# Kernel optimization log

Measured on AMD Instinct MI355X. Metric: run time of the kernel, lower is better.

The kernel has to match this reference:

```python
import jax, jax.numpy as jnp
import numpy as np

N, E, D_IN, D_OUT = 50000, 600000, 128, 128
BETA, ALPHA = 0.4, 0.6


def setup_inputs() -> dict:
    key = jax.random.key(0)
    ks = jax.random.split(key, 8)
    def xavier(k, shape):
        std = (2.0 / (shape[0] + shape[1])) ** 0.5
        return jax.random.normal(k, shape, jnp.float32) * std
    x = jax.random.normal(ks[0], (N, D_IN), jnp.float32)
    edge_index = jax.random.randint(ks[1], (2, E), 0, N, jnp.int32)
    Wq = xavier(ks[2], (D_IN, D_OUT))
    Wk = xavier(ks[3], (D_IN, D_OUT))
    Wv = xavier(ks[4], (D_IN, D_IN))
    W_gcn = xavier(ks[5], (D_IN, D_IN))   # GCNConv linear weight [out, in]
    b_gcn = jnp.zeros((D_IN,), jnp.float32)
    W_lin = xavier(ks[6], (D_OUT, D_IN))  # nn.Linear weight [out, in]
    b_lin = jnp.zeros((D_OUT,), jnp.float32)
    return {"x": x, "edge_index": edge_index, "Wq": Wq, "Wk": Wk, "Wv": Wv,
            "W_gcn": W_gcn, "b_gcn": b_gcn, "W_lin": W_lin, "b_lin": b_lin}


def gcn_conv(x, edge_index, W, b):
    # PyG GCNConv default: add self-loops, symmetric deg^-1/2 normalization.
    n = x.shape[0]
    loops = jnp.arange(n, dtype=edge_index.dtype)
    src = jnp.concatenate([edge_index[0], loops])
    dst = jnp.concatenate([edge_index[1], loops])
    deg = jax.ops.segment_sum(jnp.ones_like(dst, jnp.float32), dst, num_segments=n)
    d_inv_sqrt = jax.lax.rsqrt(deg)  # deg >= 1 thanks to self-loops
    norm = d_inv_sqrt[src] * d_inv_sqrt[dst]  # [E+N]
    xw = x @ W.T                               # [N, d]
    out = jax.ops.segment_sum(xw[src] * norm[:, None], dst, num_segments=n)
    return out + b


def reference(x, edge_index, Wq, Wk, Wv, W_gcn, b_gcn, W_lin, b_lin):
    n, d_in = x.shape
    q = x @ Wq
    q_hat = q / jnp.linalg.norm(q)  # Frobenius norm
    k = x @ Wk
    k_hat = k / jnp.linalg.norm(k)
    v = x @ Wv
    # qk = q_hat @ (k_hat^T @ 1) / in_channels  -> [n]
    qk = (q_hat @ k_hat.sum(axis=0)) / d_in
    # D = diag(1 + qk); inverse of diagonal is elementwise reciprocal
    scale = 1.0 / (1.0 + qk)
    attn = v + (q_hat @ (k_hat.T @ v)) / d_in  # [n, d_in]
    Z = BETA * scale[:, None] * attn + (1.0 - BETA) * x
    gcn = gcn_conv(x, edge_index, W_gcn, b_gcn)
    # self.dropout(gcn) result is discarded in the source -> no-op
    Z_out = (1.0 - ALPHA) * Z + ALPHA * gcn
    return Z_out @ W_lin.T + b_lin
```

## Files before the change

### kernel.cpp

```cpp
#include <hip/hip_runtime.h>
#include <hip/hip_fp16.h>
#include <cstdint>
#include <cstddef>

#define D 128
typedef unsigned short u16;
typedef short bf16x8 __attribute__((ext_vector_type(8)));
typedef float f32x4 __attribute__((ext_vector_type(4)));

__device__ __forceinline__ u16 f2b(float f) {
    uint32_t u = __float_as_uint(f);
    return (u16)((u + 0x7FFFu + ((u >> 16) & 1u)) >> 16);
}
__device__ __forceinline__ float b2f(u16 b) {
    return __uint_as_float(((uint32_t)b) << 16);
}

#define SWZ(r, k) ((k) ^ (((r) & 7) << 3))

__global__ void k_prep(const float* __restrict__ Wq, const float* __restrict__ Wk,
                       const float* __restrict__ Wv, const float* __restrict__ Wg,
                       const float* __restrict__ bg, const float* __restrict__ Wl,
                       const float* __restrict__ bl,
                       u16* __restrict__ Bcatb, float* __restrict__ biasout)
{
    const int b = blockIdx.x;
    const int t = threadIdx.x;
    if (b < 640) {
        const int strip = b >> 7, n = b & 127;
        float val;
        if (strip == 0) {
            val = Wq[t * D + n];
        } else if (strip == 1) {
            val = Wk[t * D + n];
        } else if (strip == 2) {
            float s = 0.f;
#pragma unroll 8
            for (int m = 0; m < D; ++m) s += Wv[t * D + m] * Wl[n * D + m];
            val = s;
        } else if (strip == 3) {
            val = Wl[n * D + t];
        } else {
            float s = 0.f;
#pragma unroll 8
            for (int m = 0; m < D; ++m) s += Wl[n * D + m] * Wg[m * D + t];
            val = 0.6f * s;
        }
        Bcatb[(size_t)b * D + t] = f2b(val);
    } else {
        float s = 0.f;
#pragma unroll 8
        for (int m = 0; m < D; ++m) s += bg[m] * Wl[t * D + m];
        biasout[t] = bl[t] + 0.6f * s;
    }
}

__global__ void k_init(int* __restrict__ cnt, int M)
{
    const int i = blockIdx.x * 256 + threadIdx.x;
    if (i < M) cnt[i] = 0;
}

__global__ void k_hist(const int* __restrict__ dst, int* __restrict__ cnt,
                       int* __restrict__ epos, int E)
{
    const int e = blockIdx.x * 256 + threadIdx.x;
    if (e < E) epos[e] = atomicAdd(&cnt[dst[e]], 1);
}

__global__ __launch_bounds__(1024) void k_scan1(const int* __restrict__ cnt,
                                                int* __restrict__ offs,
                                                int* __restrict__ bsum,
                                                float* __restrict__ dinv, int M)
{
    __shared__ int wsum[16];
    const int t = threadIdx.x, lane = t & 63, w = t >> 6;
    const int i = blockIdx.x * 1024 + t;
    const int v = (i < M) ? cnt[i] : 0;
    if (i < M) dinv[i] = rsqrtf((float)(v + 1));
    int s = v;
    for (int off = 1; off < 64; off <<= 1) {
        int n = __shfl_up(s, off);
        if (lane >= off) s += n;
    }
    if (lane == 63) wsum[w] = s;
    __syncthreads();
    if (w == 0) {
        int ss = (lane < 16) ? wsum[lane] : 0;
        for (int off = 1; off < 16; off <<= 1) {
            int n = __shfl_up(ss, off);
            if (lane >= off) ss += n;
        }
        if (lane < 16) wsum[lane] = ss;
    }
    __syncthreads();
    const int woff = (w == 0) ? 0 : wsum[w - 1];
    if (i < M) offs[i] = woff + s - v;
    if (t == 1023) bsum[blockIdx.x] = wsum[15];
}

__global__ void k_scanB(int* __restrict__ bsum, int nb)
{
    const int t = threadIdx.x;
    int v = (t < nb) ? bsum[t] : 0;
    int s = v;
    for (int off = 1; off < 64; off <<= 1) {
        int n = __shfl_up(s, off);
        if (t >= off) s += n;
    }
    if (t < nb) bsum[t] = s - v;
}

__global__ void k_scan2(const int* __restrict__ bsum, int* __restrict__ offs, int M)
{
    const int i = blockIdx.x * 256 + threadIdx.x;
    if (i < M) offs[i] += bsum[i >> 10];
}

__global__ void k_fill(const int* __restrict__ src, const int* __restrict__ dst,
                       const int* __restrict__ epos,
                       const float* __restrict__ dinv,
                       const int* __restrict__ offs,
                       uint32_t* __restrict__ cpk, int E)
{
    const int e = blockIdx.x * 256 + threadIdx.x;
    if (e < E) {
        const int s = src[e], d = dst[e];
        const int pos = offs[d] + epos[e];
        const float w = dinv[s] * dinv[d];
        const u16 hb = __half_as_ushort(__float2half(w));
        cpk[pos] = (uint32_t)(u16)s | ((uint32_t)hb << 16);
    }
}

__global__ __launch_bounds__(256) void k_gemm5(const float* __restrict__ x,
                                               const u16* __restrict__ Bcatb,
                                               u16* __restrict__ outbase,
                                               int M, size_t NQ)
{
    __shared__ u16 As[64 * D];
    __shared__ u16 Bs[64 * D];
    const int t = threadIdx.x;
    const int row0 = blockIdx.x * 64;
    const int n0 = blockIdx.y * 64;

#pragma unroll
    for (int p = 0; p < 4; ++p) {
        const int flat = t + 256 * p;
        const int r = flat >> 4, kg = flat & 15;
        int gr = row0 + r; if (gr > M - 1) gr = M - 1;
        const float4 f0 = *(const float4*)(x + (size_t)gr * D + kg * 8);
        const float4 f1 = *(const float4*)(x + (size_t)gr * D + kg * 8 + 4);
        u16 rr[8] = {f2b(f0.x), f2b(f0.y), f2b(f0.z), f2b(f0.w),
                     f2b(f1.x), f2b(f1.y), f2b(f1.z), f2b(f1.w)};
        *(uint4*)(As + r * D + SWZ(r, kg * 8)) = *(const uint4*)rr;
    }
#pragma unroll
    for (int p = 0; p < 4; ++p) {
        const int flat = t + 256 * p;
        const int r = flat >> 4, kg = flat & 15;
        const uint4 v = *(const uint4*)(Bcatb + (size_t)(n0 + r) * D + kg * 8);
        *(uint4*)(Bs + r * D + SWZ(r, kg * 8)) = v;
    }
    __syncthreads();

    const int lane = t & 63, w = t >> 6;
    const int wr = (w >> 1) * 32, wc = (w & 1) * 32;
    const int fr = lane & 15, kg = lane >> 4;

    f32x4 acc[2][2] = {};
#pragma unroll
    for (int ks = 0; ks < 4; ++ks) {
        const int kb = ks * 32 + kg * 8;
        bf16x8 a[2], b[2];
#pragma unroll
        for (int i = 0; i < 2; ++i) {
            const int r = wr + 16 * i + fr;
            a[i] = *(const bf16x8*)(As + r * D + SWZ(r, kb));
        }
#pragma unroll
        for (int j = 0; j < 2; ++j) {
            const int r = wc + 16 * j + fr;
            b[j] = *(const bf16x8*)(Bs + r * D + SWZ(r, kb));
        }
#pragma unroll
        for (int i = 0; i < 2; ++i)
#pragma unroll
            for (int j = 0; j < 2; ++j)
                acc[i][j] = __builtin_amdgcn_mfma_f32_16x16x32_bf16(a[i], b[j], acc[i][j], 0, 0, 0);
    }

    const int mat = n0 >> 7, col0 = n0 & 127;
    u16* outp = outbase + (size_t)mat * NQ;
#pragma unroll
    for (int i = 0; i < 2; ++i) {
#pragma unroll
        for (int reg = 0; reg < 4; ++reg) {
            const int r = row0 + wr + 16 * i + kg * 4 + reg;
            if (r < M) {
#pragma unroll
                for (int j = 0; j < 2; ++j) {
                    const int c = col0 + wc + 16 * j + fr;
                    outp[(size_t)r * D + c] = f2b(acc[i][j][reg]);
                }
            }
        }
    }
}

__global__ __launch_bounds__(256) void k_stats(const u16* __restrict__ qb,
                                               const u16* __restrict__ kb,
                                               float* __restrict__ psq,
                                               float* __restrict__ psk,
                                               float* __restrict__ pks, size_t NQ)
{
    __shared__ float lks[D];
    __shared__ float red[8];
    const int t = threadIdx.x;
    if (t < D) lks[t] = 0.f;
    __syncthreads();
    float sq = 0.f, sk = 0.f;
    float kc[8] = {0.f, 0.f, 0.f, 0.f, 0.f, 0.f, 0.f, 0.f};
    const size_t step = (size_t)gridDim.x * 256 * 8;
    const int cb = (t * 8) & 127;
    for (size_t i = ((size_t)blockIdx.x * 256 + t) * 8; i < NQ; i += step) {
        const uint4 qv = *(const uint4*)(qb + i);
        const uint4 kv = *(const uint4*)(kb + i);
        const u16* qp = (const u16*)&qv;
        const u16* kp = (const u16*)&kv;
#pragma unroll
        for (int jj = 0; jj < 8; ++jj) {
            const float q = b2f(qp[jj]); sq += q * q;
            const float k = b2f(kp[jj]); sk += k * k; kc[jj] += k;
        }
    }
#pragma unroll
    for (int jj = 0; jj < 8; ++jj) atomicAdd(&lks[cb + jj], kc[jj]);
    for (int off = 32; off > 0; off >>= 1) {
        sq += __shfl_down(sq, off);
        sk += __shfl_down(sk, off);
    }
    const int w = t >> 6;
    if ((t & 63) == 0) { red[w] = sq; red[4 + w] = sk; }
    __syncthreads();
    if (t == 0) psq[blockIdx.x] = red[0] + red[1] + red[2] + red[3];
    if (t == 64) psk[blockIdx.x] = red[4] + red[5] + red[6] + red[7];
    if (t < D) pks[(size_t)blockIdx.x * D + t] = lks[t];
}

__global__ __launch_bounds__(256) void k_ktv(const u16* __restrict__ kb,
                                             const u16* __restrict__ vWb,
                                             float* __restrict__ part, int M)
{
    __shared__ u16 kT[D * 64];
    __shared__ u16 vT[D * 64];
    const int t = threadIdx.x;
    const int P = (int)gridDim.x;
    const int chunk = (M + P - 1) / P;
    const int rbeg = blockIdx.x * chunk;
    const int rend = min(rbeg + chunk, M);

    const int lane = t & 63, w = t >> 6;
    const int fr = lane & 15, kg = lane >> 4;

    f32x4 acc[2][8] = {};

    for (int r0 = rbeg; r0 < rend; r0 += 64) {
#pragma unroll
        for (int p = 0; p < 4; ++p) {
            const int flat = t + 256 * p;
            const int rr = flat & 63, cg = flat >> 6;
            const int gr = r0 + rr;
            uint4 kv = make_uint4(0, 0, 0, 0), vv = make_uint4(0, 0, 0, 0);
            if (gr < rend) {
                kv = *(const uint4*)(kb + (size_t)gr * D + cg * 8);
                vv = *(const uint4*)(vWb + (size_t)gr * D + cg * 8);
            }
            const u16* kp = (const u16*)&kv;
            const u16* vp = (const u16*)&vv;
#pragma unroll
            for (int jj = 0; jj < 8; ++jj) {
                const int c = cg * 8 + jj;
                const int ri = rr ^ ((c & 7) << 3);
                kT[c * 64 + ri] = kp[jj];
                vT[c * 64 + ri] = vp[jj];
            }
        }
        __syncthreads();
#pragma unroll
        for (int ks = 0; ks < 2; ++ks) {
            const int rb = ks * 32 + kg * 8;
            bf16x8 a[2], b[8];
#pragma unroll
            for (int i = 0; i < 2; ++i) {
                const int m = w * 32 + 16 * i + fr;
                a[i] = *(const bf16x8*)(kT + m * 64 + (rb ^ ((m & 7) << 3)));
            }
#pragma unroll
            for (int j = 0; j < 8; ++j) {
                const int n = 16 * j + fr;
                b[j] = *(const bf16x8*)(vT + n * 64 + (rb ^ ((n & 7) << 3)));
            }
#pragma unroll
            for (int i = 0; i < 2; ++i)
#pragma unroll
                for (int j = 0; j < 8; ++j)
                    acc[i][j] = __builtin_amdgcn_mfma_f32_16x16x32_bf16(a[i], b[j], acc[i][j], 0, 0, 0);
        }
        __syncthreads();
    }
    float* pp = part + (size_t)blockIdx.x * (D * D);
#pragma unroll
    for (int i = 0; i < 2; ++i)
#pragma unroll
        for (int reg = 0; reg < 4; ++reg) {
            const int m = w * 32 + 16 * i + kg * 4 + reg;
#pragma unroll
            for (int j = 0; j < 8; ++j)
                pp[(size_t)m * D + 16 * j + fr] = acc[i][j][reg];
        }
}

__global__ void k_redC(const float* __restrict__ part, float* __restrict__ Craw, int P)
{
    const int e = blockIdx.x * 256 + threadIdx.x;
    float s0 = 0.f, s1 = 0.f, s2 = 0.f, s3 = 0.f,
          s4 = 0.f, s5 = 0.f, s6 = 0.f, s7 = 0.f;
    int p = 0;
    for (; p + 8 <= P; p += 8) {
        s0 += part[(size_t)(p + 0) * (D * D) + e];
        s1 += part[(size_t)(p + 1) * (D * D) + e];
        s2 += part[(size_t)(p + 2) * (D * D) + e];
        s3 += part[(size_t)(p + 3) * (D * D) + e];
        s4 += part[(size_t)(p + 4) * (D * D) + e];
        s5 += part[(size_t)(p + 5) * (D * D) + e];
        s6 += part[(size_t)(p + 6) * (D * D) + e];
        s7 += part[(size_t)(p + 7) * (D * D) + e];
    }
    for (; p < P; ++p) s0 += part[(size_t)p * (D * D) + e];
    Craw[e] = ((s0 + s1) + (s2 + s3)) + ((s4 + s5) + (s6 + s7));
}

__global__ __launch_bounds__(1024) void k_scalc3t(const float* __restrict__ psq,
                                                  const float* __restrict__ psk,
                                                  const float* __restrict__ pks,
                                                  const float* __restrict__ Craw,
                                                  float* __restrict__ kq,
                                                  u16* __restrict__ C3b, int NBLK)
{
    __shared__ float lpart[8][D];
    __shared__ float wred[16];
    __shared__ float invS;
    const int t = threadIdx.x;
    const int col = t & 127, grp = t >> 7;
    float s = 0.f;
#pragma unroll 8
    for (int bq = grp; bq < NBLK; bq += 8) s += pks[(size_t)bq * D + col];
    lpart[grp][col] = s;
    const int w = t >> 6, lane = t & 63;
    float v = 0.f;
    if (t < NBLK) v = psq[t];
    else if (t < 2 * NBLK) v = psk[t - NBLK];
    for (int off = 32; off > 0; off >>= 1) v += __shfl_down(v, off);
    if (lane == 0 && w < 8) wred[w] = v;
    __syncthreads();
    if (t == 0) {
        const float sq = wred[0] + wred[1] + wred[2] + wred[3];
        const float sk = wred[4] + wred[5] + wred[6] + wred[7];
        invS = 1.0f / (sqrtf(sq) * sqrtf(sk) * 128.0f);
    }
    float ks = 0.f;
    if (t < D) {
#pragma unroll
        for (int g = 0; g < 8; ++g) ks += lpart[g][t];
    }
    __syncthreads();
    const float inv = invS;
    if (t < D) kq[t] = ks * inv;
#pragma unroll
    for (int i = 0; i < 16; ++i) {
        const int e = t + 1024 * i;
        C3b[e] = f2b(Craw[(size_t)(e & 127) * D + (e >> 7)] * inv);
    }
}

__global__ __launch_bounds__(256) void k_final(const u16* __restrict__ qb,
                                               const u16* __restrict__ C3b,
                                               const u16* __restrict__ vWb,
                                               const u16* __restrict__ xWb,
                                               const u16* __restrict__ ub,
                                               const int* __restrict__ cnt,
                                               const float* __restrict__ kq,
                                               const float* __restrict__ biasout,
                                               float* __restrict__ out, int M)
{
    __shared__ u16 As[64 * D];
    __shared__ u16 Bs[D * D];
    __shared__ float scaleS[64];
    const int t = threadIdx.x;
    const int row0 = blockIdx.x * 64;

#pragma unroll
    for (int p = 0; p < 4; ++p) {
        const int flat = t + 256 * p;
        const int r = flat >> 4, kg2 = flat & 15;
        int gr = row0 + r; if (gr > M - 1) gr = M - 1;
        const uint4 v = *(const uint4*)(qb + (size_t)gr * D + kg2 * 8);
        *(uint4*)(As + r * D + SWZ(r, kg2 * 8)) = v;
    }
#pragma unroll
    for (int p = 0; p < 8; ++p) {
        const int flat = t + 256 * p;
        const int r = flat >> 4, kg2 = flat & 15;
        const uint4 v = *(const uint4*)(C3b + (size_t)r * D + kg2 * 8);
        *(uint4*)(Bs + r * D + SWZ(r, kg2 * 8)) = v;
    }
    __syncthreads();

    {
        const int rr = t >> 2, qq = t & 3;
        float s = 0.f;
#pragma unroll
        for (int i = 0; i < 4; ++i) {
            const int kk = qq * 32 + i * 8;
            const bf16x8 a = *(const bf16x8*)(As + rr * D + SWZ(rr, kk));
            const u16* ap = (const u16*)&a;
#pragma unroll
            for (int jj = 0; jj < 8; ++jj) s += b2f(ap[jj]) * kq[kk + jj];
        }
        s += __shfl_xor(s, 1);
        s += __shfl_xor(s, 2);
        if (qq == 0) scaleS[rr] = 0.16f / (1.0f + s);
    }

    const int lane = t & 63, w = t >> 6;
    const int fr = lane & 15, kg = lane >> 4;

    f32x4 acc[8] = {};
#pragma unroll
    for (int ks = 0; ks < 4; ++ks) {
        const int kb2 = ks * 32 + kg * 8;
        const int r = w * 16 + fr;
        const bf16x8 a = *(const bf16x8*)(As + r * D + SWZ(r, kb2));
#pragma unroll
        for (int j = 0; j < 8; ++j) {
            const int n = 16 * j + fr;
            const bf16x8 b = *(const bf16x8*)(Bs + n * D + SWZ(n, kb2));
            acc[j] = __builtin_amdgcn_mfma_f32_16x16x32_bf16(a, b, acc[j], 0, 0, 0);
        }
    }
    __syncthreads();

#pragma unroll
    for (int reg = 0; reg < 4; ++reg) {
        const int rr = w * 16 + kg * 4 + reg;
        const int r = row0 + rr;
        if (r < M) {
            const float rc = scaleS[rr];
            const float sc = 1.0f / (float)(cnt[r] + 1);
#pragma unroll
            for (int j = 0; j < 8; ++j) {
                const int c = 16 * j + fr;
                const size_t idx = (size_t)r * D + c;
                out[idx] = rc * (b2f(vWb[idx]) + acc[j][reg]) + 0.24f * b2f(xWb[idx])
                         + biasout[c] + sc * b2f(ub[idx]);
            }
        }
    }
}

__global__ __launch_bounds__(256) void k_gather(const int* __restrict__ offs,
                                                const int* __restrict__ cnt,
                                                const uint32_t* __restrict__ cpk,
                                                const u16* __restrict__ ub,
                                                float* __restrict__ out, int M)
{
    const int t = threadIdx.x;
    const int w = t >> 6, lane = t & 63;
    const int d = blockIdx.x * 4 + w;
    if (d >= M) return;
    const int g = lane >> 4, sub = lane & 15;
    const int beg = offs[d];
    const int n = cnt[d];
    if (n == 0) return;
    const int end = beg + n;
    float acc[8] = {};
    for (int j0 = beg; j0 < end; j0 += 8) {
        const int j1 = j0 + g, j2 = j0 + 4 + g;
        int s1 = 0, s2 = 0;
        float w1 = 0.f, w2 = 0.f;
        if (j1 < end) {
            const uint32_t p = cpk[j1];
            s1 = (int)(p & 0xFFFFu);
            w1 = __half2float(__ushort_as_half((u16)(p >> 16)));
        }
        if (j2 < end) {
            const uint32_t p = cpk[j2];
            s2 = (int)(p & 0xFFFFu);
            w2 = __half2float(__ushort_as_half((u16)(p >> 16)));
        }
        const uint4 r1 = *(const uint4*)(ub + (size_t)s1 * D + sub * 8);
        const uint4 r2 = *(const uint4*)(ub + (size_t)s2 * D + sub * 8);
        const u16* p1 = (const u16*)&r1;
        const u16* p2 = (const u16*)&r2;
#pragma unroll
        for (int i = 0; i < 8; ++i) acc[i] += w1 * b2f(p1[i]) + w2 * b2f(p2[i]);
    }
#pragma unroll
    for (int i = 0; i < 8; ++i) {
        acc[i] += __shfl_xor(acc[i], 16);
        acc[i] += __shfl_xor(acc[i], 32);
    }
    if (g == 0) {
        float* o = out + (size_t)d * D + sub * 8;
        float4 o0 = *(float4*)o, o1 = *(float4*)(o + 4);
        o0.x += acc[0]; o0.y += acc[1]; o0.z += acc[2]; o0.w += acc[3];
        o1.x += acc[4]; o1.y += acc[5]; o1.z += acc[6]; o1.w += acc[7];
        *(float4*)o = o0; *(float4*)(o + 4) = o1;
    }
}

extern "C" void kernel_launch(void* const* d_in, const int* in_sizes, int n_in,
                              void* d_out, int out_size, void* d_ws, size_t ws_size,
                              hipStream_t stream)
{
    const float* x  = (const float*)d_in[0];
    const int*   ei = (const int*)d_in[1];
    const float* Wq = (const float*)d_in[2];
    const float* Wk = (const float*)d_in[3];
    const float* Wv = (const float*)d_in[4];
    const float* Wg = (const float*)d_in[5];
    const float* bg = (const float*)d_in[6];
    const float* Wl = (const float*)d_in[7];
    const float* bl = (const float*)d_in[8];

    const int M = in_sizes[0] / D;
    const int E = in_sizes[1] / 2;
    const size_t NQ = (size_t)M * D;
    const int P = 192;
    const int SB = 256;
    const int NB = (M + 1023) / 1024;

    char* base = (char*)d_ws;
    auto alloc = [&](size_t bytes) -> char* {
        char* p = base; base += (bytes + 63) & ~(size_t)63; return p;
    };
    float* part    = (float*)alloc((size_t)P * D * D * 4);
    float* Craw    = (float*)alloc(D * D * 4);
    float* dinv    = (float*)alloc((size_t)M * 4);
    float* psq     = (float*)alloc(SB * 4);
    float* psk     = (float*)alloc(SB * 4);
    float* pks     = (float*)alloc((size_t)SB * D * 4);
    float* kq      = (float*)alloc(D * 4);
    float* biasout = (float*)alloc(D * 4);
    int*   cnt     = (int*)alloc((size_t)M * 4);
    int*   offs    = (int*)alloc((size_t)M * 4);
    int*   bsum    = (int*)alloc(64 * 4);
    int*   epos    = (int*)alloc((size_t)E * 4);
    uint32_t* cpk  = (uint32_t*)alloc((size_t)E * 4);
    u16*   Bcatb   = (u16*)alloc((size_t)640 * D * 2);
    u16*   C3b     = (u16*)alloc(D * D * 2);
    u16*   qb      = (u16*)alloc(NQ * 2);
    u16*   kb      = (u16*)alloc(NQ * 2);
    u16*   vWb     = (u16*)alloc(NQ * 2);
    u16*   xWb     = (u16*)alloc(NQ * 2);
    u16*   ub      = (u16*)alloc(NQ * 2);
    (void)kb; (void)vWb; (void)xWb;

    float* out = (float*)d_out;

    k_prep<<<dim3(641), dim3(128), 0, stream>>>(Wq, Wk, Wv, Wg, bg, Wl, bl, Bcatb, biasout);
    k_init<<<(M + 255) / 256, 256, 0, stream>>>(cnt, M);
    k_hist<<<(E + 255) / 256, 256, 0, stream>>>(ei + E, cnt, epos, E);
    k_scan1<<<NB, 1024, 0, stream>>>(cnt, offs, bsum, dinv, M);
    k_scanB<<<1, 64, 0, stream>>>(bsum, NB);
    k_scan2<<<(M + 255) / 256, 256, 0, stream>>>(bsum, offs, M);
    k_fill<<<(E + 255) / 256, 256, 0, stream>>>(ei, ei + E, epos, dinv, offs, cpk, E);

    k_gemm5<<<dim3((M + 63) / 64, 10), 256, 0, stream>>>(x, Bcatb, qb, M, NQ);
    k_stats<<<SB, 256, 0, stream>>>(qb, kb, psq, psk, pks, NQ);
    k_ktv<<<P, 256, 0, stream>>>(kb, vWb, part, M);
    k_redC<<<64, 256, 0, stream>>>(part, Craw, P);
    k_scalc3t<<<1, 1024, 0, stream>>>(psq, psk, pks, Craw, kq, C3b, SB);

    k_final<<<(M + 63) / 64, 256, 0, stream>>>(qb, C3b, vWb, xWb, ub, cnt, kq, biasout, out, M);
    k_gather<<<(M + 3) / 4, 256, 0, stream>>>(offs, cnt, cpk, ub, out, M);
}
```

Before: 208.4 us.

## Fuse Q/K norm stats into projection GEMM and loop all column tiles per block

The projection GEMM now launches one block per 64-row tile. Each block loops over all ten 64-column chunks of the concatenated weight matrix, double-buffering the weight tiles in shared memory, so the x tile is loaded and converted once instead of ten times. The Frobenius-norm sums and K column sums are accumulated in the GEMM epilogue, with shared atomics for the column sums. That removes the separate stats kernel and its re-read of q and k. The tradeoffs are fewer, longer blocks with more shared memory and serialized column work, shared-atomic contention, and a final reduction over many more per-block partials.

```diff
diff --git a/kernel.cpp b/kernel.cpp
--- a/kernel.cpp
+++ b/kernel.cpp
@@ -136,13 +136,19 @@
 __global__ __launch_bounds__(256) void k_gemm5(const float* __restrict__ x,
                                                const u16* __restrict__ Bcatb,
                                                u16* __restrict__ outbase,
+                                               float* __restrict__ psq,
+                                               float* __restrict__ psk,
+                                               float* __restrict__ pks,
                                                int M, size_t NQ)
 {
     __shared__ u16 As[64 * D];
-    __shared__ u16 Bs[64 * D];
+    __shared__ u16 Bs[2][64 * D];
+    __shared__ float lks[D];
+    __shared__ float red[8];
     const int t = threadIdx.x;
     const int row0 = blockIdx.x * 64;
-    const int n0 = blockIdx.y * 64;
+
+    if (t < D) lks[t] = 0.f;
 
 #pragma unroll
     for (int p = 0; p < 4; ++p) {
@@ -159,88 +165,84 @@
     for (int p = 0; p < 4; ++p) {
         const int flat = t + 256 * p;
         const int r = flat >> 4, kg = flat & 15;
-        const uint4 v = *(const uint4*)(Bcatb + (size_t)(n0 + r) * D + kg * 8);
-        *(uint4*)(Bs + r * D + SWZ(r, kg * 8)) = v;
+        const uint4 v = *(const uint4*)(Bcatb + (size_t)r * D + kg * 8);
+        *(uint4*)(Bs[0] + r * D + SWZ(r, kg * 8)) = v;
     }
     __syncthreads();
 
     const int lane = t & 63, w = t >> 6;
     const int wr = (w >> 1) * 32, wc = (w & 1) * 32;
-    const int fr = lane & 15, kg = lane >> 4;
-
-    f32x4 acc[2][2] = {};
-#pragma unroll
-    for (int ks = 0; ks < 4; ++ks) {
-        const int kb = ks * 32 + kg * 8;
-        bf16x8 a[2], b[2];
+    const int fr = lane & 15, kg2 = lane >> 4;
+
+    float sq = 0.f, sk = 0.f;
+
+    for (int c = 0; c < 10; ++c) {
+        const int cur = c & 1;
+        if (c < 9) {
+#pragma unroll
+            for (int p = 0; p < 4; ++p) {
+                const int flat = t + 256 * p;
+                const int r = flat >> 4, kg = flat & 15;
+                const uint4 v = *(const uint4*)(Bcatb + (size_t)((c + 1) * 64 + r) * D + kg * 8);
+                *(uint4*)(Bs[cur ^ 1] + r * D + SWZ(r, kg * 8)) = v;
+            }
+        }
+
+        f32x4 acc[2][2] = {};
+#pragma unroll
+        for (int ks = 0; ks < 4; ++ks) {
+            const int kb = ks * 32 + kg2 * 8;
+            bf16x8 a[2], b[2];
+#pragma unroll
+            for (int i = 0; i < 2; ++i) {
+                const int r = wr + 16 * i + fr;
+                a[i] = *(const bf16x8*)(As + r * D + SWZ(r, kb));
+            }
+#pragma unroll
+            for (int j = 0; j < 2; ++j) {
+                const int r = wc + 16 * j + fr;
+                b[j] = *(const bf16x8*)(Bs[cur] + r * D + SWZ(r, kb));
+            }
+#pragma unroll
+            for (int i = 0; i < 2; ++i)
+#pragma unroll
+                for (int j = 0; j < 2; ++j)
+                    acc[i][j] = __builtin_amdgcn_mfma_f32_16x16x32_bf16(a[i], b[j], acc[i][j], 0, 0, 0);
+        }
+
+        const int mat = c >> 1, col0 = (c & 1) * 64;
+        u16* outp = outbase + (size_t)mat * NQ;
 #pragma unroll
         for (int i = 0; i < 2; ++i) {
-            const int r = wr + 16 * i + fr;
-            a[i] = *(const bf16x8*)(As + r * D + SWZ(r, kb));
-        }
-#pragma unroll
-        for (int j = 0; j < 2; ++j) {
-            const int r = wc + 16 * j + fr;
-            b[j] = *(const bf16x8*)(Bs + r * D + SWZ(r, kb));
-        }
-#pragma unroll
-        for (int i = 0; i < 2; ++i)
-#pragma unroll
-            for (int j = 0; j < 2; ++j)
-                acc[i][j] = __builtin_amdgcn_mfma_f32_16x16x32_bf16(a[i], b[j], acc[i][j], 0, 0, 0);
-    }
-
-    const int mat = n0 >> 7, col0 = n0 & 127;
-    u16* outp = outbase + (size_t)mat * NQ;
-#pragma unroll
-    for (int i = 0; i < 2; ++i) {
-#pragma unroll
-        for (int reg = 0; reg < 4; ++reg) {
-            const int r = row0 + wr + 16 * i + kg * 4 + reg;
-            if (r < M) {
-#pragma unroll
-                for (int j = 0; j < 2; ++j) {
-                    const int c = col0 + wc + 16 * j + fr;
-                    outp[(size_t)r * D + c] = f2b(acc[i][j][reg]);
+#pragma unroll
+            for (int reg = 0; reg < 4; ++reg) {
+                const int r = row0 + wr + 16 * i + kg2 * 4 + reg;
+                if (r < M) {
+#pragma unroll
+                    for (int j = 0; j < 2; ++j) {
+                        const int col = col0 + wc + 16 * j + fr;
+                        const u16 hv = f2b(acc[i][j][reg]);
+                        outp[(size_t)r * D + col] = hv;
+                        if (c < 4) {
+                            const float v = b2f(hv);
+                            if (c < 2) {
+                                sq += v * v;
+                            } else {
+                                sk += v * v;
+                                atomicAdd(&lks[col], v);
+                            }
+                        }
+                    }
                 }
             }
         }
-    }
-}
-
-__global__ __launch_bounds__(256) void k_stats(const u16* __restrict__ qb,
-                                               const u16* __restrict__ kb,
-                                               float* __restrict__ psq,
-                                               float* __restrict__ psk,
-                                               float* __restrict__ pks, size_t NQ)
-{
-    __shared__ float lks[D];
-    __shared__ float red[8];
-    const int t = threadIdx.x;
-    if (t < D) lks[t] = 0.f;
-    __syncthreads();
-    float sq = 0.f, sk = 0.f;
-    float kc[8] = {0.f, 0.f, 0.f, 0.f, 0.f, 0.f, 0.f, 0.f};
-    const size_t step = (size_t)gridDim.x * 256 * 8;
-    const int cb = (t * 8) & 127;
-    for (size_t i = ((size_t)blockIdx.x * 256 + t) * 8; i < NQ; i += step) {
-        const uint4 qv = *(const uint4*)(qb + i);
-        const uint4 kv = *(const uint4*)(kb + i);
-        const u16* qp = (const u16*)&qv;
-        const u16* kp = (const u16*)&kv;
-#pragma unroll
-        for (int jj = 0; jj < 8; ++jj) {
-            const float q = b2f(qp[jj]); sq += q * q;
-            const float k = b2f(kp[jj]); sk += k * k; kc[jj] += k;
-        }
-    }
-#pragma unroll
-    for (int jj = 0; jj < 8; ++jj) atomicAdd(&lks[cb + jj], kc[jj]);
+        __syncthreads();
+    }
+
     for (int off = 32; off > 0; off >>= 1) {
         sq += __shfl_down(sq, off);
         sk += __shfl_down(sk, off);
     }
-    const int w = t >> 6;
     if ((t & 63) == 0) { red[w] = sq; red[4 + w] = sk; }
     __syncthreads();
     if (t == 0) psq[blockIdx.x] = red[0] + red[1] + red[2] + red[3];
@@ -349,7 +351,8 @@
                                                   u16* __restrict__ C3b, int NBLK)
 {
     __shared__ float lpart[8][D];
-    __shared__ float wred[16];
+    __shared__ float wredA[16];
+    __shared__ float wredB[16];
     __shared__ float invS;
     const int t = threadIdx.x;
     const int col = t & 127, grp = t >> 7;
@@ -358,15 +361,18 @@
     for (int bq = grp; bq < NBLK; bq += 8) s += pks[(size_t)bq * D + col];
     lpart[grp][col] = s;
     const int w = t >> 6, lane = t & 63;
-    float v = 0.f;
-    if (t < NBLK) v = psq[t];
-    else if (t < 2 * NBLK) v = psk[t - NBLK];
-    for (int off = 32; off > 0; off >>= 1) v += __shfl_down(v, off);
-    if (lane == 0 && w < 8) wred[w] = v;
+    float a = (t < NBLK) ? psq[t] : 0.f;
+    float b = (t < NBLK) ? psk[t] : 0.f;
+    for (int off = 32; off > 0; off >>= 1) {
+        a += __shfl_down(a, off);
+        b += __shfl_down(b, off);
+    }
+    if (lane == 0) { wredA[w] = a; wredB[w] = b; }
     __syncthreads();
     if (t == 0) {
-        const float sq = wred[0] + wred[1] + wred[2] + wred[3];
-        const float sk = wred[4] + wred[5] + wred[6] + wred[7];
+        float sq = 0.f, sk = 0.f;
+#pragma unroll
+        for (int i = 0; i < 16; ++i) { sq += wredA[i]; sk += wredB[i]; }
         invS = 1.0f / (sqrtf(sq) * sqrtf(sk) * 128.0f);
     }
     float ks = 0.f;
@@ -538,7 +544,7 @@
     const int E = in_sizes[1] / 2;
     const size_t NQ = (size_t)M * D;
     const int P = 192;
-    const int SB = 256;
+    const int NBG = (M + 63) / 64;
     const int NB = (M + 1023) / 1024;
 
     char* base = (char*)d_ws;
@@ -548,9 +554,9 @@
     float* part    = (float*)alloc((size_t)P * D * D * 4);
     float* Craw    = (float*)alloc(D * D * 4);
     float* dinv    = (float*)alloc((size_t)M * 4);
-    float* psq     = (float*)alloc(SB * 4);
-    float* psk     = (float*)alloc(SB * 4);
-    float* pks     = (float*)alloc((size_t)SB * D * 4);
+    float* psq     = (float*)alloc((size_t)NBG * 4);
+    float* psk     = (float*)alloc((size_t)NBG * 4);
+    float* pks     = (float*)alloc((size_t)NBG * D * 4);
     float* kq      = (float*)alloc(D * 4);
     float* biasout = (float*)alloc(D * 4);
     int*   cnt     = (int*)alloc((size_t)M * 4);
@@ -577,11 +583,10 @@
     k_scan2<<<(M + 255) / 256, 256, 0, stream>>>(bsum, offs, M);
     k_fill<<<(E + 255) / 256, 256, 0, stream>>>(ei, ei + E, epos, dinv, offs, cpk, E);
 
-    k_gemm5<<<dim3((M + 63) / 64, 10), 256, 0, stream>>>(x, Bcatb, qb, M, NQ);
-    k_stats<<<SB, 256, 0, stream>>>(qb, kb, psq, psk, pks, NQ);
+    k_gemm5<<<NBG, 256, 0, stream>>>(x, Bcatb, qb, psq, psk, pks, M, NQ);
     k_ktv<<<P, 256, 0, stream>>>(kb, vWb, part, M);
     k_redC<<<64, 256, 0, stream>>>(part, Craw, P);
-    k_scalc3t<<<1, 1024, 0, stream>>>(psq, psk, pks, Craw, kq, C3b, SB);
+    k_scalc3t<<<1, 1024, 0, stream>>>(psq, psk, pks, Craw, kq, C3b, NBG);
 
     k_final<<<(M + 63) / 64, 256, 0, stream>>>(qb, C3b, vWb, xWb, ub, cnt, kq, biasout, out, M);
     k_gather<<<(M + 3) / 4, 256, 0, stream>>>(offs, cnt, cpk, ub, out, M);
```

Measured after the change: 223.7 us. 7.4% more time.
